# Kernel tuning notes

Measured on AMD Instinct MI355X. Metric: run time of the kernel, lower is better.

## Reference

```python
import jax, jax.numpy as jnp
import numpy as np

D_MODEL = 1024
N_HEAD = 16
EPS = 1e-11  # non-standard: masked scores are set to eps BEFORE softmax (not -inf)


def setup_inputs() -> dict:
    key = jax.random.key(0)
    ks = jax.random.split(key, 12)
    B, S, D = 4, 2048, D_MODEL
    s = 1.0 / np.sqrt(D)
    return {
        "query": jax.random.normal(ks[0], (B, S, D), dtype=jnp.float32),
        "key": jax.random.normal(ks[1], (B, S, D), dtype=jnp.float32),
        "value": jax.random.normal(ks[2], (B, S, D), dtype=jnp.float32),
        "mask": jax.random.randint(ks[3], (B, S, S), 0, 2, dtype=jnp.int32),
        "wq": jax.random.normal(ks[4], (D, D), dtype=jnp.float32) * s,
        "bq": jnp.zeros((D,), dtype=jnp.float32),
        "wk": jax.random.normal(ks[5], (D, D), dtype=jnp.float32) * s,
        "bk": jnp.zeros((D,), dtype=jnp.float32),
        "wv": jax.random.normal(ks[6], (D, D), dtype=jnp.float32) * s,
        "bv": jnp.zeros((D,), dtype=jnp.float32),
        "wo": jax.random.normal(ks[7], (D, D), dtype=jnp.float32) * s,
        "bo": jnp.zeros((D,), dtype=jnp.float32),
    }


def reference(query, key, value, mask, wq, bq, wk, bk, wv, bv, wo, bo):
    B, S, D = query.shape
    H = N_HEAD
    dk = D // H
    # QKV projections (nn.Linear: x @ W.T + b)
    q = query @ wq.T + bq
    k = key @ wk.T + bk
    v = value @ wv.T + bv
    # [B, S, D] -> [B, H, S, dk]
    q = q.reshape(B, S, H, dk).transpose(0, 2, 1, 3)
    k = k.reshape(B, S, H, dk).transpose(0, 2, 1, 3)
    v = v.reshape(B, S, H, dk).transpose(0, 2, 1, 3)
    # scaled dot-product scores [B, H, S, S]
    scores = jnp.einsum("bhqd,bhkd->bhqk", q, k) / jnp.sqrt(jnp.float32(dk))
    # faithful quirk: fill masked positions with eps (not -inf)
    m = mask[:, None, :, :]  # [B, 1, S, S]
    scores = jnp.where(m == 0, jnp.float32(EPS), scores)
    attn = jax.nn.softmax(scores, axis=-1)
    out = jnp.einsum("bhqk,bhkd->bhqd", attn, v)
    out = out.transpose(0, 2, 1, 3).reshape(B, S, D)
    return out @ wo.T + bo
```

## Files before the change

kernel.cpp:

```cpp
#include <hip/hip_runtime.h>

typedef __attribute__((ext_vector_type(8))) short short8;
typedef __attribute__((ext_vector_type(4))) float floatx4;
typedef __attribute__((ext_vector_type(16))) float floatx16;
typedef __attribute__((ext_vector_type(4))) unsigned int uintx4;

__device__ inline unsigned short f2bf(float f) {
    union { float f; unsigned int i; } c; c.f = f;
    unsigned int x = c.i;
    unsigned int r = x + 0x7fffu + ((x >> 16) & 1u);
    return (unsigned short)(r >> 16);
}

__device__ inline unsigned int pk_bf16(float lo, float hi) {
    unsigned int r;
    asm("v_cvt_pk_bf16_f32 %0, %1, %2" : "=v"(r) : "v"(lo), "v"(hi));
    return r;
}

__device__ inline float ex2(float x) {
#if __has_builtin(__builtin_amdgcn_exp2f)
    return __builtin_amdgcn_exp2f(x);
#else
    return exp2f(x);
#endif
}

__device__ inline void plane_swap(unsigned int& a, unsigned int& b) {
#if __has_builtin(__builtin_amdgcn_permlane32_swap)
    auto r = __builtin_amdgcn_permlane32_swap(a, b, false, false);
    a = r[0]; b = r[1];
#else
    int lane = threadIdx.x & 63;
    unsigned int tb = (unsigned int)__shfl_xor((int)b, 32, 64);
    unsigned int ta = (unsigned int)__shfl_xor((int)a, 32, 64);
    unsigned int na = (lane < 32) ? a : tb;
    unsigned int nb = (lane < 32) ? ta : b;
    a = na; b = nb;
#endif
}

__device__ inline void gl_lds16(const unsigned short* g, unsigned short* lds_uniform) {
    __builtin_amdgcn_global_load_lds(
        (const __attribute__((address_space(1))) void*)g,
        (__attribute__((address_space(3))) void*)lds_uniform,
        16, 0, 0);
}

__global__ void cvt_bf16(const float* __restrict__ in, unsigned short* __restrict__ out, int n8)
{
    int i = blockIdx.x * blockDim.x + threadIdx.x;
    if (i < n8) {
        const float4* p = (const float4*)(in + (size_t)i * 8);
        float4 a = p[0], b = p[1];
        short8 v;
        v[0] = (short)f2bf(a.x); v[1] = (short)f2bf(a.y);
        v[2] = (short)f2bf(a.z); v[3] = (short)f2bf(a.w);
        v[4] = (short)f2bf(b.x); v[5] = (short)f2bf(b.y);
        v[6] = (short)f2bf(b.z); v[7] = (short)f2bf(b.w);
        *(short8*)(out + (size_t)i * 8) = v;
    }
}

__global__ void cvt_bf16_3(const float* __restrict__ i0, const float* __restrict__ i1,
                           const float* __restrict__ i2,
                           unsigned short* __restrict__ o0, unsigned short* __restrict__ o1,
                           unsigned short* __restrict__ o2, int n8)
{
    const int w = blockIdx.y;
    const float* in = (w == 0) ? i0 : (w == 1) ? i1 : i2;
    unsigned short* out = (w == 0) ? o0 : (w == 1) ? o1 : o2;
    int i = blockIdx.x * blockDim.x + threadIdx.x;
    if (i < n8) {
        const float4* p = (const float4*)(in + (size_t)i * 8);
        float4 a = p[0], b = p[1];
        short8 v;
        v[0] = (short)f2bf(a.x); v[1] = (short)f2bf(a.y);
        v[2] = (short)f2bf(a.z); v[3] = (short)f2bf(a.w);
        v[4] = (short)f2bf(b.x); v[5] = (short)f2bf(b.y);
        v[6] = (short)f2bf(b.z); v[7] = (short)f2bf(b.w);
        *(short8*)(out + (size_t)i * 8) = v;
    }
}

__global__ void mask_pack(const int* __restrict__ m, unsigned short* __restrict__ o, int n16)
{
    int i = blockIdx.x * blockDim.x + threadIdx.x;
    if (i < n16) {
        const int4* p = (const int4*)(m + (size_t)i * 16);
        unsigned int bits = 0;
#pragma unroll
        for (int j = 0; j < 4; j++) {
            int4 v = p[j];
            bits |= (v.x != 0 ? 1u : 0u) << (j * 4 + 0);
            bits |= (v.y != 0 ? 1u : 0u) << (j * 4 + 1);
            bits |= (v.z != 0 ? 1u : 0u) << (j * 4 + 2);
            bits |= (v.w != 0 ? 1u : 0u) << (j * 4 + 3);
        }
        o[i] = (unsigned short)bits;
    }
}

__global__ __launch_bounds__(256, 2)
void gemm_bt(const unsigned short* __restrict__ A,
             const unsigned short* __restrict__ W,
             const float* __restrict__ bias,
             void* __restrict__ outv,
             int M, int N, int K, int mode)
{
    __shared__ __align__(16) unsigned short As[128 * 64];
    __shared__ __align__(16) unsigned short Bs[128 * 64];
    const int t = threadIdx.x, lane = t & 63, wv = t >> 6;
    const int quad = lane >> 4, l16 = lane & 15;
    const int m0 = blockIdx.x * 128, n0 = blockIdx.y * 128;
    const int wm = (wv >> 1) * 64, wn = (wv & 1) * 64;

    floatx4 acc[4][4] = {};

    for (int k0 = 0; k0 < K; k0 += 64) {
#pragma unroll
        for (int s = 0; s < 4; s++) {
            int e = t + s * 256;
            int row = e >> 3, slot = e & 7;
            int chunk = slot ^ (row & 7);
            gl_lds16(&A[(size_t)(m0 + row) * K + k0 + chunk * 8], &As[wv * 512 + s * 2048]);
            gl_lds16(&W[(size_t)(n0 + row) * K + k0 + chunk * 8], &Bs[wv * 512 + s * 2048]);
        }
        asm volatile("s_waitcnt vmcnt(0)" ::: "memory");
        __syncthreads();

        short8 af[4][2], bfr[4][2];
#pragma unroll
        for (int i = 0; i < 4; i++)
#pragma unroll
            for (int c = 0; c < 2; c++)
                af[i][c] = *(const short8*)&As[(wm + i * 16 + l16) * 64 + (((c * 4 + quad) ^ (l16 & 7)) * 8)];
#pragma unroll
        for (int j = 0; j < 4; j++)
#pragma unroll
            for (int c = 0; c < 2; c++)
                bfr[j][c] = *(const short8*)&Bs[(wn + j * 16 + l16) * 64 + (((c * 4 + quad) ^ (l16 & 7)) * 8)];

#pragma unroll
        for (int c = 0; c < 2; c++)
#pragma unroll
            for (int i = 0; i < 4; i++)
#pragma unroll
                for (int j = 0; j < 4; j++)
                    acc[i][j] = __builtin_amdgcn_mfma_f32_16x16x32_bf16(af[i][c], bfr[j][c], acc[i][j], 0, 0, 0);
        __syncthreads();
    }

#pragma unroll
    for (int i = 0; i < 4; i++) {
#pragma unroll
        for (int j = 0; j < 4; j++) {
            int n = n0 + wn + j * 16 + l16;
            float bv = bias[n];
#pragma unroll
            for (int r = 0; r < 4; r++) {
                int m = m0 + wm + i * 16 + quad * 4 + r;
                float v = acc[i][j][r] + bv;
                if (mode == 2) {
                    ((float*)outv)[(size_t)m * N + n] = v;
                } else {
                    int b = m >> 11, s = m & 2047, h = n >> 6, d = n & 63;
                    size_t idx = (mode == 0)
                        ? (((size_t)b * 16 + h) * 2048 + s) * 64 + d
                        : (((size_t)b * 16 + h) * 64 + d) * 2048 + s;
                    ((unsigned short*)outv)[idx] = f2bf(v);
                }
            }
        }
    }
}

__global__ __launch_bounds__(256, 4)
void attn(const unsigned short* __restrict__ qb,
          const unsigned short* __restrict__ kb,
          const unsigned short* __restrict__ vtb,
          const unsigned char* __restrict__ mb,
          unsigned short* __restrict__ ob)
{
    __shared__ __align__(16) unsigned short Ks[2][64 * 64];
    __shared__ __align__(16) unsigned short Vs[2][64 * 64];
    const int t = threadIdx.x, lane = t & 63, wv = t >> 6;
    const int hi = lane >> 5, l31 = lane & 31;
    const int bh = blockIdx.x & 63;
    const int b = bh >> 4, h = bh & 15;
    const int q0 = (blockIdx.x >> 6) * 128;
    const size_t kvbase = (size_t)bh * 2048 * 64;
    const float K1 = 0.1803368801f;
    const float K2 = -14.4269504089f;
    const float PM = 4.5399931e-05f;

    const int qr = q0 + wv * 32 + l31;

    short8 qf[4];
#pragma unroll
    for (int g = 0; g < 4; g++)
        qf[g] = *(const short8*)&qb[kvbase + (size_t)qr * 64 + g * 16 + hi * 8];

    const uint2* mrowp = (const uint2*)(mb + ((size_t)b * 2048 + qr) * 256);
    uint2 mcur = mrowp[0];

    floatx16 O[2] = {};
    float lrun = 0.f;

#pragma unroll
    for (int s = 0; s < 2; s++) {
        int e = t + s * 256;
        int row = e >> 3, slot = e & 7, chunk = slot ^ (row & 7);
        gl_lds16(&kb[kvbase + (size_t)row * 64 + chunk * 8], &Ks[0][wv * 512 + s * 2048]);
        gl_lds16(&vtb[kvbase + (size_t)row * 2048 + chunk * 8], &Vs[0][wv * 512 + s * 2048]);
    }

    for (int kt = 0; kt < 2048; kt += 64) {
        const int cur = (kt >> 6) & 1;
        asm volatile("s_waitcnt vmcnt(0)" ::: "memory");
        __syncthreads();

        uint2 mnext = mcur;
        if (kt + 64 < 2048) {
#pragma unroll
            for (int s = 0; s < 2; s++) {
                int e = t + s * 256;
                int row = e >> 3, slot = e & 7, chunk = slot ^ (row & 7);
                gl_lds16(&kb[kvbase + (size_t)(kt + 64 + row) * 64 + chunk * 8],
                         &Ks[cur ^ 1][wv * 512 + s * 2048]);
                gl_lds16(&vtb[kvbase + (size_t)row * 2048 + (kt + 64) + chunk * 8],
                         &Vs[cur ^ 1][wv * 512 + s * 2048]);
            }
            mnext = mrowp[(kt >> 6) + 1];
        }

#pragma unroll
        for (int c32 = 0; c32 < 2; c32++) {
            const int krow = c32 * 32 + l31;
            short8 kf[4];
#pragma unroll
            for (int g = 0; g < 4; g++)
                kf[g] = *(const short8*)&Ks[cur][krow * 64 + (((g * 2 + hi) ^ (krow & 7)) * 8)];

            floatx16 C = {};
#pragma unroll
            for (int g = 0; g < 4; g++)
                C = __builtin_amdgcn_mfma_f32_32x32x16_bf16(kf[g], qf[g], C, 0, 0, 0);

            unsigned int w = (c32 ? mcur.y : mcur.x) >> (hi * 4);
            float p[16];
            float rs = 0.f;
#pragma unroll
            for (int r = 0; r < 16; r++) {
                float e_ = ex2(fmaf(C[r], K1, K2));
                unsigned int bit = (w >> ((r & 3) + 8 * (r >> 2))) & 1u;
                p[r] = bit ? e_ : PM;
                rs += p[r];
            }
            lrun += rs;

            unsigned int s_[8];
#pragma unroll
            for (int i = 0; i < 8; i++) s_[i] = pk_bf16(p[2 * i], p[2 * i + 1]);
            plane_swap(s_[0], s_[2]); plane_swap(s_[1], s_[3]);
            plane_swap(s_[4], s_[6]); plane_swap(s_[5], s_[7]);
            short8 fragA = __builtin_bit_cast(short8, (uintx4){s_[0], s_[1], s_[2], s_[3]});
            short8 fragB = __builtin_bit_cast(short8, (uintx4){s_[4], s_[5], s_[6], s_[7]});

#pragma unroll
            for (int dt = 0; dt < 2; dt++) {
                const int vrow = dt * 32 + l31;
                short8 vA = *(const short8*)&Vs[cur][vrow * 64 + (((c32 * 4 + hi) ^ (vrow & 7)) * 8)];
                short8 vB = *(const short8*)&Vs[cur][vrow * 64 + (((c32 * 4 + 2 + hi) ^ (vrow & 7)) * 8)];
                O[dt] = __builtin_amdgcn_mfma_f32_32x32x16_bf16(vA, fragA, O[dt], 0, 0, 0);
                O[dt] = __builtin_amdgcn_mfma_f32_32x32x16_bf16(vB, fragB, O[dt], 0, 0, 0);
            }
        }
        mcur = mnext;
        __syncthreads();
    }

    float l = lrun + __shfl_xor(lrun, 32, 64);
    float inv = 1.0f / l;
#pragma unroll
    for (int dt = 0; dt < 2; dt++)
#pragma unroll
        for (int g = 0; g < 4; g++) {
            int d0 = dt * 32 + 8 * g + 4 * hi;
            unsigned int w0 = pk_bf16(O[dt][4 * g + 0] * inv, O[dt][4 * g + 1] * inv);
            unsigned int w1 = pk_bf16(O[dt][4 * g + 2] * inv, O[dt][4 * g + 3] * inv);
            uint2 ww; ww.x = w0; ww.y = w1;
            *(uint2*)&ob[((size_t)b * 2048 + qr) * 1024 + h * 64 + d0] = ww;
        }
}

extern "C" void kernel_launch(void* const* d_in, const int* in_sizes, int n_in,
                              void* d_out, int out_size, void* d_ws, size_t ws_size,
                              hipStream_t stream)
{
    const float* query = (const float*)d_in[0];
    const float* key   = (const float*)d_in[1];
    const float* value = (const float*)d_in[2];
    const int*   mask  = (const int*)d_in[3];
    const float* wq = (const float*)d_in[4];
    const float* bq = (const float*)d_in[5];
    const float* wk = (const float*)d_in[6];
    const float* bk = (const float*)d_in[7];
    const float* wv = (const float*)d_in[8];
    const float* bv = (const float*)d_in[9];
    const float* wo = (const float*)d_in[10];
    const float* bo = (const float*)d_in[11];

    char* ws = (char*)d_ws;
    const size_t T = 16777216;
    unsigned short* S0 = (unsigned short*)(ws);
    unsigned short* S1 = (unsigned short*)(ws + T);
    unsigned short* S2 = (unsigned short*)(ws + 2 * T);
    unsigned short* D0 = (unsigned short*)d_out;
    unsigned short* WQ = (unsigned short*)((char*)d_out + T);
    unsigned short* WK = (unsigned short*)((char*)d_out + T + 2097152);
    unsigned short* WV = (unsigned short*)((char*)d_out + T + 2 * 2097152);
    unsigned short* MB = (unsigned short*)((char*)d_out + T + 3 * 2097152);

    dim3 g(64, 8);

    cvt_bf16_3<<<dim3(512, 3), 256, 0, stream>>>(wq, wk, wv, WQ, WK, WV, 131072);
    mask_pack<<<dim3(4096), 256, 0, stream>>>(mask, MB, 1048576);

    cvt_bf16<<<dim3(4096), 256, 0, stream>>>(query, S0, 1048576);
    gemm_bt<<<g, 256, 0, stream>>>(S0, WQ, bq, S1, 8192, 1024, 1024, 0);
    cvt_bf16<<<dim3(4096), 256, 0, stream>>>(key, S0, 1048576);
    gemm_bt<<<g, 256, 0, stream>>>(S0, WK, bk, S2, 8192, 1024, 1024, 0);
    cvt_bf16<<<dim3(4096), 256, 0, stream>>>(value, S0, 1048576);
    gemm_bt<<<g, 256, 0, stream>>>(S0, WV, bv, D0, 8192, 1024, 1024, 1);

    attn<<<dim3(1024), 256, 0, stream>>>(S1, S2, D0, (const unsigned char*)MB, S0);

    cvt_bf16<<<dim3(512), 256, 0, stream>>>(wo, S1, 131072);
    gemm_bt<<<g, 256, 0, stream>>>(S0, S1, bo, d_out, 8192, 1024, 1024, 2);
}
```

Baseline: 426.2 us.

## Fuse fp32-to-bf16 activation conversion into QKV GEMM loads and merge prep kernels

The QKV projection GEMMs now read fp32 activations directly, convert them to bf16 in registers and store them into LDS. This removes three standalone conversion kernels and their round trip of bf16 intermediates through global memory. The weight conversion and mask packing are also merged into one launch. In exchange, the A-tile load is now a synchronous register path instead of a direct global-to-LDS load, and it reads twice the bytes per tile, which could slow the GEMM main loop.

```diff
diff --git a/kernel.cpp b/kernel.cpp
--- a/kernel.cpp
+++ b/kernel.cpp
@@ -62,16 +62,18 @@
     }
 }
 
-__global__ void cvt_bf16_3(const float* __restrict__ i0, const float* __restrict__ i1,
-                           const float* __restrict__ i2,
-                           unsigned short* __restrict__ o0, unsigned short* __restrict__ o1,
-                           unsigned short* __restrict__ o2, int n8)
-{
-    const int w = blockIdx.y;
-    const float* in = (w == 0) ? i0 : (w == 1) ? i1 : i2;
-    unsigned short* out = (w == 0) ? o0 : (w == 1) ? o1 : o2;
-    int i = blockIdx.x * blockDim.x + threadIdx.x;
-    if (i < n8) {
+__global__ void prep(const float* __restrict__ wq, const float* __restrict__ wk,
+                     const float* __restrict__ wv,
+                     unsigned short* __restrict__ oq, unsigned short* __restrict__ ok,
+                     unsigned short* __restrict__ ov,
+                     const int* __restrict__ m, unsigned short* __restrict__ om)
+{
+    const int bid = blockIdx.x, t = threadIdx.x;
+    if (bid < 1536) {
+        const int w = bid >> 9;
+        const float* in = (w == 0) ? wq : (w == 1) ? wk : wv;
+        unsigned short* out = (w == 0) ? oq : (w == 1) ? ok : ov;
+        int i = (bid & 511) * 256 + t;
         const float4* p = (const float4*)(in + (size_t)i * 8);
         float4 a = p[0], b = p[1];
         short8 v;
@@ -80,13 +82,8 @@
         v[4] = (short)f2bf(b.x); v[5] = (short)f2bf(b.y);
         v[6] = (short)f2bf(b.z); v[7] = (short)f2bf(b.w);
         *(short8*)(out + (size_t)i * 8) = v;
-    }
-}
-
-__global__ void mask_pack(const int* __restrict__ m, unsigned short* __restrict__ o, int n16)
-{
-    int i = blockIdx.x * blockDim.x + threadIdx.x;
-    if (i < n16) {
+    } else {
+        int i = (bid - 1536) * 256 + t;
         const int4* p = (const int4*)(m + (size_t)i * 16);
         unsigned int bits = 0;
 #pragma unroll
@@ -97,16 +94,16 @@
             bits |= (v.z != 0 ? 1u : 0u) << (j * 4 + 2);
             bits |= (v.w != 0 ? 1u : 0u) << (j * 4 + 3);
         }
-        o[i] = (unsigned short)bits;
+        om[i] = (unsigned short)bits;
     }
 }
 
 __global__ __launch_bounds__(256, 2)
-void gemm_bt(const unsigned short* __restrict__ A,
+void gemm_bt(const void* __restrict__ Av,
              const unsigned short* __restrict__ W,
              const float* __restrict__ bias,
              void* __restrict__ outv,
-             int M, int N, int K, int mode)
+             int M, int N, int K, int mode, int acvt)
 {
     __shared__ __align__(16) unsigned short As[128 * 64];
     __shared__ __align__(16) unsigned short Bs[128 * 64];
@@ -114,6 +111,8 @@
     const int quad = lane >> 4, l16 = lane & 15;
     const int m0 = blockIdx.x * 128, n0 = blockIdx.y * 128;
     const int wm = (wv >> 1) * 64, wn = (wv & 1) * 64;
+    const unsigned short* Ab = (const unsigned short*)Av;
+    const float* Af = (const float*)Av;
 
     floatx4 acc[4][4] = {};
 
@@ -123,8 +122,30 @@
             int e = t + s * 256;
             int row = e >> 3, slot = e & 7;
             int chunk = slot ^ (row & 7);
-            gl_lds16(&A[(size_t)(m0 + row) * K + k0 + chunk * 8], &As[wv * 512 + s * 2048]);
             gl_lds16(&W[(size_t)(n0 + row) * K + k0 + chunk * 8], &Bs[wv * 512 + s * 2048]);
+        }
+        if (acvt) {
+#pragma unroll
+            for (int s = 0; s < 4; s++) {
+                int e = t + s * 256;
+                int row = e >> 3, slot = e & 7;
+                int chunk = slot ^ (row & 7);
+                const float* src = Af + (size_t)(m0 + row) * K + k0 + chunk * 8;
+                float4 a0 = ((const float4*)src)[0];
+                float4 a1 = ((const float4*)src)[1];
+                uintx4 pk;
+                pk[0] = pk_bf16(a0.x, a0.y); pk[1] = pk_bf16(a0.z, a0.w);
+                pk[2] = pk_bf16(a1.x, a1.y); pk[3] = pk_bf16(a1.z, a1.w);
+                *(uintx4*)&As[s * 2048 + wv * 512 + lane * 8] = pk;
+            }
+        } else {
+#pragma unroll
+            for (int s = 0; s < 4; s++) {
+                int e = t + s * 256;
+                int row = e >> 3, slot = e & 7;
+                int chunk = slot ^ (row & 7);
+                gl_lds16(&Ab[(size_t)(m0 + row) * K + k0 + chunk * 8], &As[wv * 512 + s * 2048]);
+            }
         }
         asm volatile("s_waitcnt vmcnt(0)" ::: "memory");
         __syncthreads();
@@ -324,18 +345,14 @@
 
     dim3 g(64, 8);
 
-    cvt_bf16_3<<<dim3(512, 3), 256, 0, stream>>>(wq, wk, wv, WQ, WK, WV, 131072);
-    mask_pack<<<dim3(4096), 256, 0, stream>>>(mask, MB, 1048576);
-
-    cvt_bf16<<<dim3(4096), 256, 0, stream>>>(query, S0, 1048576);
-    gemm_bt<<<g, 256, 0, stream>>>(S0, WQ, bq, S1, 8192, 1024, 1024, 0);
-    cvt_bf16<<<dim3(4096), 256, 0, stream>>>(key, S0, 1048576);
-    gemm_bt<<<g, 256, 0, stream>>>(S0, WK, bk, S2, 8192, 1024, 1024, 0);
-    cvt_bf16<<<dim3(4096), 256, 0, stream>>>(value, S0, 1048576);
-    gemm_bt<<<g, 256, 0, stream>>>(S0, WV, bv, D0, 8192, 1024, 1024, 1);
+    prep<<<dim3(5632), 256, 0, stream>>>(wq, wk, wv, WQ, WK, WV, mask, MB);
+
+    gemm_bt<<<g, 256, 0, stream>>>(query, WQ, bq, S1, 8192, 1024, 1024, 0, 1);
+    gemm_bt<<<g, 256, 0, stream>>>(key,   WK, bk, S2, 8192, 1024, 1024, 0, 1);
+    gemm_bt<<<g, 256, 0, stream>>>(value, WV, bv, D0, 8192, 1024, 1024, 1, 1);
 
     attn<<<dim3(1024), 256, 0, stream>>>(S1, S2, D0, (const unsigned char*)MB, S0);
 
     cvt_bf16<<<dim3(512), 256, 0, stream>>>(wo, S1, 131072);
-    gemm_bt<<<g, 256, 0, stream>>>(S0, S1, bo, d_out, 8192, 1024, 1024, 2);
-}
+    gemm_bt<<<g, 256, 0, stream>>>(S0, S1, bo, d_out, 8192, 1024, 1024, 2, 0);
+}
```

Measured after the change: 497.2 us. 16.7% more time.
